# Kernel tuning notes

Hardware: AMD Instinct MI355X
Metric: run time of the kernel (lower is better)

The kernel has to match this reference:

```python
import jax, jax.numpy as jnp
import numpy as np

B, L, D = 4, 2048, 2048
NH, HD, K = 32, 64, 16
LR = 1.0
EPS = 1e-6


def ln_fwd(x, gamma, beta):
    mu = x.mean(-1, keepdims=True)
    var = jnp.var(x, axis=-1, keepdims=True)
    x_hat = (x - mu) / jnp.sqrt(var + EPS)
    return gamma * x_hat + beta


def ln_fused_l2_bwd(x, target, gamma, beta):
    # grad of 0.5*||LN(x)-target||^2 wrt x (matches LayerNormFunction.backward
    # with grad_output = LN(x) - target)
    d = x.shape[-1]
    mu = x.mean(-1, keepdims=True)
    var = jnp.var(x, axis=-1, keepdims=True)
    std = jnp.sqrt(var + EPS)
    x_hat = (x - mu) / std
    y = gamma * x_hat + beta
    g = (y - target) * gamma
    return (d * g - g.sum(-1, keepdims=True) - x_hat * (g * x_hat).sum(-1, keepdims=True)) / (d * std)


def setup_inputs() -> dict:
    key = jax.random.key(0)
    ks = jax.random.split(key, 12)
    s = 0.02
    return {
        "hidden_states": jax.random.normal(ks[0], (B, L, D), jnp.float32),
        "Wq": jax.random.normal(ks[1], (D, D), jnp.float32) * s,
        "Wk": jax.random.normal(ks[2], (D, D), jnp.float32) * s,
        "Wv": jax.random.normal(ks[3], (D, D), jnp.float32) * s,
        "Wo": jax.random.normal(ks[4], (D, D), jnp.float32) * s,
        "linear_weight": jax.random.normal(ks[5], (NH, 1, D), jnp.float32) * s,
        "linear_bias": jnp.zeros((NH, 1), jnp.float32),
        "ln_weight": jnp.ones((NH, HD), jnp.float32),
        "ln_bias": jnp.zeros((NH, HD), jnp.float32),
        "W1_init": jax.random.normal(ks[6], (NH, HD, HD), jnp.float32) * s,
        "b1_init": jnp.zeros((NH, 1, HD), jnp.float32),
    }


def reference(hidden_states, Wq, Wk, Wv, Wo, linear_weight, linear_bias,
              ln_weight, ln_bias, W1_init, b1_init):
    Bq, Lq, Dq = hidden_states.shape
    n_chunk = Lq // K

    def split(x):  # [B,L,D] -> [B,NH,n_chunk,K,HD]
        return x.reshape(Bq, n_chunk, K, NH, HD).transpose(0, 3, 1, 2, 4)

    XC = split(hidden_states @ Wq.T)
    XB = split(hidden_states @ Wk.T)
    XA = split(hidden_states @ Wv.T)

    # inner-loop learning-rate coefficient: [B,NH,n_chunk,K,1]
    X = hidden_states.reshape(Bq, n_chunk, K, Dq)
    ilr = jnp.einsum('bnkd,hd->bhnk', X, linear_weight[:, 0, :]) + linear_bias[:, 0][None, :, None, None]
    ilr_gated = jax.nn.sigmoid(ilr)[..., None]
    token_idx = 1.0 / jnp.arange(1, K + 1, dtype=hidden_states.dtype)
    coeff = (LR * token_idx).reshape(1, 1, 1, K, 1) * ilr_gated / HD

    ln_w = ln_weight.reshape(1, NH, 1, HD)
    ln_b = ln_bias.reshape(1, NH, 1, HD)
    mask = jnp.tril(jnp.ones((K, K), hidden_states.dtype))

    W1 = jnp.broadcast_to(W1_init[None], (Bq, NH, HD, HD))
    b1 = jnp.broadcast_to(b1_init[None], (Bq, NH, 1, HD))

    def step(carry, inp):
        W1, b1 = carry
        xc, xb, xa, co = inp  # [B,NH,K,HD], co: [B,NH,K,1]
        Z1 = xb @ W1 + b1
        grad = ln_fused_l2_bwd(Z1, xa - xb, ln_w, ln_b)  # [B,NH,K,HD]
        Attn = mask * jnp.einsum('bhkf,bhjf->bhkj', xc, xb)
        E = mask * co.transpose(0, 1, 3, 2)  # E[i,j] = coeff_j * (j<=i)
        b1_bar = b1 - E @ grad
        Z1_bar = xc @ W1 - (Attn * E) @ grad + b1_bar
        W1_new = W1 - jnp.einsum('bhkf,bhkg->bhfg', co * xb, grad)
        b1_new = b1 - (co * grad).sum(-2, keepdims=True)
        out = xc + ln_fwd(Z1_bar, ln_w, ln_b)
        return (W1_new, b1_new), out

    xs = (XC.transpose(2, 0, 1, 3, 4), XB.transpose(2, 0, 1, 3, 4),
          XA.transpose(2, 0, 1, 3, 4), coeff.transpose(2, 0, 1, 3, 4))
    (_, _), outs = jax.lax.scan(step, (W1, b1), xs)
    # outs: [n_chunk,B,NH,K,HD] -> [B,L,D]
    XCW = outs.transpose(1, 0, 3, 2, 4).reshape(Bq, Lq, Dq)
    return XCW @ Wo.T
```

## Files before the change

kernel.cpp:

```cpp
#include <hip/hip_runtime.h>


typedef __attribute__((ext_vector_type(4))) float float4v;
typedef __attribute__((ext_vector_type(2))) float float2v;
typedef __attribute__((ext_vector_type(8))) __bf16 bf16x8;
typedef __attribute__((ext_vector_type(4))) short short4v;
typedef __attribute__((ext_vector_type(4))) unsigned int uint4v;
typedef __attribute__((ext_vector_type(2))) unsigned int uint2v;

__device__ __forceinline__ unsigned short f2bf(float f) {
  unsigned int u = __builtin_bit_cast(unsigned int, f);
  u += 0x7FFFu + ((u >> 16) & 1u);
  return (unsigned short)(u >> 16);
}
__device__ __forceinline__ float bf2f(unsigned short s) {
  unsigned int u = ((unsigned int)s) << 16;
  return __builtin_bit_cast(float, u);
}
__device__ __forceinline__ void lds_load16(const void* g, void* l) {
  __builtin_amdgcn_global_load_lds((const __attribute__((address_space(1))) void*)g,
                                   (__attribute__((address_space(3))) void*)l, 16, 0, 0);
}

__device__ __forceinline__ void store_out(float* p, float v) { *p = v; }
__device__ __forceinline__ void store_out(unsigned short* p, float v) { *p = f2bf(v); }

template <int CTRL>
__device__ __forceinline__ float dppmov(float x) {
  return __builtin_bit_cast(
      float, __builtin_amdgcn_update_dpp(0, __builtin_bit_cast(int, x), CTRL, 0xF, 0xF, true));
}
__device__ __forceinline__ float red16(float x) {
  x += dppmov<0xB1>(x);
  x += dppmov<0x4E>(x);
  x += dppmov<0x124>(x);
  x += dppmov<0x128>(x);
  return x;
}
__device__ __forceinline__ unsigned int cvtpk_bf16(float lo, float hi) {
  unsigned int r;
  asm("v_cvt_pk_bf16_f32 %0, %1, %2" : "=v"(r) : "v"(lo), "v"(hi));
  return r;
}
__device__ __forceinline__ void bar_sync() {
  asm volatile("s_waitcnt lgkmcnt(0)" ::: "memory");
  __builtin_amdgcn_s_barrier();
  asm volatile("" ::: "memory");
}

template <typename OUT>
__global__ __launch_bounds__(256) void gemm_bt(
    const unsigned short* __restrict__ A, const unsigned short* __restrict__ B,
    OUT* __restrict__ C, int M, int N, int K) {
  __shared__ unsigned short sA[128 * 32];
  __shared__ unsigned short sB[128 * 32];
  const int tid = threadIdx.x;
  const int wave = tid >> 6;
  const int lane = tid & 63;
  const int quad = lane >> 4;
  const int l15 = lane & 15;
  const int wm = (wave >> 1) * 64;
  const int wn = (wave & 1) * 64;
  const int bm = blockIdx.y * 128;
  const int bn = blockIdx.x * 128;

  float4v acc[4][4];
#pragma unroll
  for (int i = 0; i < 4; ++i)
#pragma unroll
    for (int j = 0; j < 4; ++j) acc[i][j] = (float4v){0.f, 0.f, 0.f, 0.f};

  const int srow = tid >> 2;
  const int scol = (tid & 3) * 8;
  const unsigned short* aptr = A + (size_t)(bm + srow) * K + scol;
  const unsigned short* bptr = B + (size_t)(bn + srow) * K + scol;
  unsigned short* sAw0 = &sA[wave * 512];
  unsigned short* sAw1 = &sA[2048 + wave * 512];
  unsigned short* sBw0 = &sB[wave * 512];
  unsigned short* sBw1 = &sB[2048 + wave * 512];
  const size_t astep = (size_t)64 * K;

  for (int kt = 0; kt < K; kt += 32) {
    __syncthreads();
    lds_load16(aptr + kt, sAw0);
    lds_load16(aptr + kt + astep, sAw1);
    lds_load16(bptr + kt, sBw0);
    lds_load16(bptr + kt + astep, sBw1);
    __syncthreads();
    bf16x8 af[4], bf[4];
#pragma unroll
    for (int i = 0; i < 4; ++i)
      af[i] = *(const bf16x8*)&sA[(wm + i * 16 + l15) * 32 + quad * 8];
#pragma unroll
    for (int j = 0; j < 4; ++j)
      bf[j] = *(const bf16x8*)&sB[(wn + j * 16 + l15) * 32 + quad * 8];
#pragma unroll
    for (int i = 0; i < 4; ++i)
#pragma unroll
      for (int j = 0; j < 4; ++j)
        acc[i][j] = __builtin_amdgcn_mfma_f32_16x16x32_bf16(af[i], bf[j], acc[i][j], 0, 0, 0);
  }

#pragma unroll
  for (int i = 0; i < 4; ++i) {
    const int row0 = bm + wm + i * 16 + quad * 4;
#pragma unroll
    for (int j = 0; j < 4; ++j) {
      const int col = bn + wn + j * 16 + l15;
#pragma unroll
      for (int r = 0; r < 4; ++r)
        store_out(&C[(size_t)(row0 + r) * N + col], acc[i][j][r]);
    }
  }
}

__global__ __launch_bounds__(256) void f32_to_bf16_k(const float* __restrict__ s,
                                                     unsigned short* __restrict__ d, int n) {
  const int i = (blockIdx.x * 256 + threadIdx.x) * 8;
  if (i >= n) return;
  const float4v a = *(const float4v*)(s + i);
  const float4v b = *(const float4v*)(s + i + 4);
  uint4v o;
  o[0] = (unsigned int)f2bf(a[0]) | ((unsigned int)f2bf(a[1]) << 16);
  o[1] = (unsigned int)f2bf(a[2]) | ((unsigned int)f2bf(a[3]) << 16);
  o[2] = (unsigned int)f2bf(b[0]) | ((unsigned int)f2bf(b[1]) << 16);
  o[3] = (unsigned int)f2bf(b[2]) | ((unsigned int)f2bf(b[3]) << 16);
  *(uint4v*)(d + i) = o;
}

__global__ __launch_bounds__(256) void coeff_k(const unsigned short* __restrict__ ilr,
                                               const float* __restrict__ lb,
                                               float* __restrict__ coeff) {
  const int gid = blockIdx.x * 256 + threadIdx.x;
  const int row = gid >> 5;
  const int h = gid & 31;
  const float v = bf2f(ilr[row * 128 + h]) + lb[h];
  const float sig = 1.0f / (1.0f + __expf(-v));
  const int b = row >> 11;
  const int pos = row & 2047;
  const int cc = pos >> 4;
  const int k = pos & 15;
  coeff[((((size_t)b * 32 + h) * 128 + cc) << 4) + k] = sig / (64.0f * (float)(k + 1));
}

__global__ __launch_bounds__(256, 1) void ttt_scan(
    const unsigned short* __restrict__ XC, const unsigned short* __restrict__ XB,
    const unsigned short* __restrict__ XA, const float* __restrict__ coeff,
    const float* __restrict__ lnw, const float* __restrict__ lnb,
    const float* __restrict__ W1i, const float* __restrict__ b1i,
    unsigned short* __restrict__ XCW) {
  const int b = blockIdx.x >> 5;
  const int h = blockIdx.x & 31;
  const int tid = threadIdx.x;
  const int wave = tid >> 6;
  const int lane = tid & 63;
  const int quad = lane >> 4;
  const int l15 = lane & 15;

  constexpr int LDW = 88;
  __shared__ __attribute__((aligned(16))) unsigned short sXC[2][16 * LDW];
  __shared__ __attribute__((aligned(16))) unsigned short sXB[2][16 * LDW];
  __shared__ __attribute__((aligned(16))) unsigned short sXA[2][16 * LDW];
  __shared__ __attribute__((aligned(16))) unsigned short sW1[64 * LDW];
  __shared__ __attribute__((aligned(16))) float sRed[3][16][8];

  const int fcol = wave * 16 + l15;
  const float gam = lnw[h * 64 + fcol];
  const float bet = lnb[h * 64 + fcol];

  float4v W1r[4];
#pragma unroll
  for (int mt = 0; mt < 4; ++mt) {
    float4v v;
#pragma unroll
    for (int r = 0; r < 4; ++r)
      v[r] = W1i[(size_t)h * 4096 + (size_t)(mt * 16 + quad * 4 + r) * 64 + fcol];
    W1r[mt] = v;
  }
  float b1v = b1i[h * 64 + fcol];

#pragma unroll
  for (int mt = 0; mt < 4; ++mt) {
    uint2v p;
    p[0] = cvtpk_bf16(W1r[mt][0], W1r[mt][1]);
    p[1] = cvtpk_bf16(W1r[mt][2], W1r[mt][3]);
    *(uint2v*)&sW1[(size_t)fcol * LDW + mt * 16 + quad * 4] = p;
  }

  const int u = tid & 127;
  const int grow = u >> 3;
  const int gcol = (u & 7) * 8;
  const size_t hdoff = (size_t)h * 64;
  const size_t browoff = (size_t)b * 2048;
  const float* cobase = coeff + (((size_t)b * 32 + h) * 128) * 16;
  const float inv64 = 1.0f / 64.0f;
  const float4v zero4 = {0.f, 0.f, 0.f, 0.f};

  uint4v pA = {0, 0, 0, 0}, pB = {0, 0, 0, 0};
  float4v pcof;
  {
    const size_t goff = (browoff + (size_t)grow) * 2048 + hdoff + gcol;
    if (tid < 128) {
      pA = *(const uint4v*)(XC + goff);
      pB = *(const uint4v*)(XA + goff);
    } else {
      pA = *(const uint4v*)(XB + goff);
    }
    pcof = *(const float4v*)(cobase + quad * 4);
  }

  for (int c = 0; c < 128; ++c) {
    const int buf = c & 1;
    if (tid < 128) {
      *(uint4v*)&sXC[buf][grow * LDW + gcol] = pA;
      *(uint4v*)&sXA[buf][grow * LDW + gcol] = pB;
    } else {
      *(uint4v*)&sXB[buf][grow * LDW + gcol] = pA;
    }
    const float4v cof = pcof;
    bar_sync();

    {
      const int cn = (c < 127) ? c + 1 : 127;
      const size_t goff = (browoff + (size_t)(cn * 16 + grow)) * 2048 + hdoff + gcol;
      if (tid < 128) {
        pA = *(const uint4v*)(XC + goff);
        pB = *(const uint4v*)(XA + goff);
      } else {
        pA = *(const uint4v*)(XB + goff);
      }
      pcof = *(const float4v*)(cobase + (size_t)cn * 16 + quad * 4);
    }

    bf16x8 xbf[2], xcf[2], w1f[2];
#pragma unroll
    for (int hh = 0; hh < 2; ++hh) {
      xbf[hh] = *(const bf16x8*)&sXB[buf][l15 * LDW + hh * 32 + quad * 8];
      xcf[hh] = *(const bf16x8*)&sXC[buf][l15 * LDW + hh * 32 + quad * 8];
      w1f[hh] = *(const bf16x8*)&sW1[(size_t)fcol * LDW + hh * 32 + quad * 8];
    }

    float4v z = __builtin_amdgcn_mfma_f32_16x16x32_bf16(xbf[0], w1f[0], zero4, 0, 0, 0);
    z = __builtin_amdgcn_mfma_f32_16x16x32_bf16(xbf[1], w1f[1], z, 0, 0, 0);
#pragma unroll
    for (int r = 0; r < 4; ++r) z[r] += b1v;

    float s1p[4], s2p[4];
#pragma unroll
    for (int r = 0; r < 4; ++r) {
      s1p[r] = red16(z[r]);
      s2p[r] = red16(z[r] * z[r]);
    }
    if (l15 == 0) {
#pragma unroll
      for (int r = 0; r < 4; ++r)
        *(float2v*)&sRed[0][quad * 4 + r][wave * 2] = (float2v){s1p[r], s2p[r]};
    }

    float4v at = __builtin_amdgcn_mfma_f32_16x16x32_bf16(xbf[0], xcf[0], zero4, 0, 0, 0);
    at = __builtin_amdgcn_mfma_f32_16x16x32_bf16(xbf[1], xcf[1], at, 0, 0, 0);

    bar_sync();

    float mu[4], rstd[4];
#pragma unroll
    for (int r = 0; r < 4; ++r) {
      const float4v v0 = *(const float4v*)&sRed[0][quad * 4 + r][0];
      const float4v v1 = *(const float4v*)&sRed[0][quad * 4 + r][4];
      const float s1 = v0[0] + v0[2] + v1[0] + v1[2];
      const float s2 = v0[1] + v0[3] + v1[1] + v1[3];
      mu[r] = s1 * inv64;
      rstd[r] = rsqrtf(s2 * inv64 - mu[r] * mu[r] + 1e-6f);
    }
    float xh[4], gg[4];
#pragma unroll
    for (int r = 0; r < 4; ++r) {
      xh[r] = (z[r] - mu[r]) * rstd[r];
      const int toff = (quad * 4 + r) * LDW + fcol;
      const float tgt = bf2f(sXA[buf][toff]) - bf2f(sXB[buf][toff]);
      gg[r] = (gam * xh[r] + bet - tgt) * gam;
    }
    float sgp[4], sgxp[4];
#pragma unroll
    for (int r = 0; r < 4; ++r) {
      sgp[r] = red16(gg[r]);
      sgxp[r] = red16(gg[r] * xh[r]);
    }
    if (l15 == 0) {
#pragma unroll
      for (int r = 0; r < 4; ++r)
        *(float2v*)&sRed[1][quad * 4 + r][wave * 2] = (float2v){sgp[r], sgxp[r]};
    }

    short4v caf[4];
#pragma unroll
    for (int mt = 0; mt < 4; ++mt)
#pragma unroll
      for (int jj = 0; jj < 4; ++jj)
        caf[mt][jj] =
            (short)f2bf(-cof[jj] * bf2f(sXB[buf][(quad * 4 + jj) * LDW + mt * 16 + l15]));
    short4v m1f;
#pragma unroll
    for (int jj = 0; jj < 4; ++jj) {
      const int k = quad * 4 + jj;
      const float e = (k <= l15) ? cof[jj] : 0.0f;
      m1f[jj] = (short)f2bf(-(at[jj] + 1.0f) * e);
    }

    bar_sync();

    float grad[4];
    short4v gradb;
#pragma unroll
    for (int r = 0; r < 4; ++r) {
      const float4v v0 = *(const float4v*)&sRed[1][quad * 4 + r][0];
      const float4v v1 = *(const float4v*)&sRed[1][quad * 4 + r][4];
      const float sg = v0[0] + v0[2] + v1[0] + v1[2];
      const float sgx = v0[1] + v0[3] + v1[1] + v1[3];
      grad[r] = (64.0f * gg[r] - sg - xh[r] * sgx) * (rstd[r] * inv64);
      gradb[r] = (short)f2bf(grad[r]);
    }

    float4v zb = __builtin_amdgcn_mfma_f32_16x16x32_bf16(xcf[0], w1f[0], zero4, 0, 0, 0);
    zb = __builtin_amdgcn_mfma_f32_16x16x32_bf16(xcf[1], w1f[1], zb, 0, 0, 0);
    zb = __builtin_amdgcn_mfma_f32_16x16x16bf16_1k(m1f, gradb, zb, 0, 0, 0);
#pragma unroll
    for (int r = 0; r < 4; ++r) zb[r] += b1v;

#pragma unroll
    for (int r = 0; r < 4; ++r) {
      s1p[r] = red16(zb[r]);
      s2p[r] = red16(zb[r] * zb[r]);
    }
    if (l15 == 0) {
#pragma unroll
      for (int r = 0; r < 4; ++r)
        *(float2v*)&sRed[2][quad * 4 + r][wave * 2] = (float2v){s1p[r], s2p[r]};
    }

    {
      float pb = cof[0] * grad[0] + cof[1] * grad[1] + cof[2] * grad[2] + cof[3] * grad[3];
      pb += __shfl_xor(pb, 16);
      pb += __shfl_xor(pb, 32);
      b1v -= pb;
    }
#pragma unroll
    for (int mt = 0; mt < 4; ++mt)
      W1r[mt] = __builtin_amdgcn_mfma_f32_16x16x16bf16_1k(caf[mt], gradb, W1r[mt], 0, 0, 0);

    bar_sync();

#pragma unroll
    for (int r = 0; r < 4; ++r) {
      const float4v v0 = *(const float4v*)&sRed[2][quad * 4 + r][0];
      const float4v v1 = *(const float4v*)&sRed[2][quad * 4 + r][4];
      const float s1 = v0[0] + v0[2] + v1[0] + v1[2];
      const float s2 = v0[1] + v0[3] + v1[1] + v1[3];
      const float mu2 = s1 * inv64;
      const float rstd2 = rsqrtf(s2 * inv64 - mu2 * mu2 + 1e-6f);
      const float xhat = (zb[r] - mu2) * rstd2;
      const float y = gam * xhat + bet;
      const float o = bf2f(sXC[buf][(quad * 4 + r) * LDW + fcol]) + y;
      XCW[(browoff + (size_t)(c * 16 + quad * 4 + r)) * 2048 + hdoff + fcol] = f2bf(o);
    }

#pragma unroll
    for (int mt = 0; mt < 4; ++mt) {
      uint2v p;
      p[0] = cvtpk_bf16(W1r[mt][0], W1r[mt][1]);
      p[1] = cvtpk_bf16(W1r[mt][2], W1r[mt][3]);
      *(uint2v*)&sW1[(size_t)fcol * LDW + mt * 16 + quad * 4] = p;
    }
  }
}

extern "C" void kernel_launch(void* const* d_in, const int* in_sizes, int n_in,
                              void* d_out, int out_size, void* d_ws, size_t ws_size,
                              hipStream_t stream) {
  const float* hs = (const float*)d_in[0];
  const float* Wq = (const float*)d_in[1];
  const float* Wk = (const float*)d_in[2];
  const float* Wv = (const float*)d_in[3];
  const float* Wo = (const float*)d_in[4];
  const float* lw = (const float*)d_in[5];
  const float* lb = (const float*)d_in[6];
  const float* lnw = (const float*)d_in[7];
  const float* lnb = (const float*)d_in[8];
  const float* W1i = (const float*)d_in[9];
  const float* b1i = (const float*)d_in[10];
  float* out = (float*)d_out;
  char* ws = (char*)d_ws;

  unsigned short* hsb = (unsigned short*)(ws);
  unsigned short* wqb = (unsigned short*)(ws + 33554432);
  unsigned short* wkb = (unsigned short*)(ws + 41943040);
  unsigned short* wvb = (unsigned short*)(ws + 50331648);
  unsigned short* wob = (unsigned short*)(ws + 58720256);
  unsigned short* lwb = (unsigned short*)(ws + 67108864);
  unsigned short* XCb = (unsigned short*)(ws + 67633152);
  unsigned short* XBb = (unsigned short*)(ws + 101187584);
  unsigned short* XAb = (unsigned short*)(ws + 134742016);
  unsigned short* ilrb = (unsigned short*)(ws + 168296448);
  float* coeff = (float*)(ws + 170393600);

  f32_to_bf16_k<<<8192, 256, 0, stream>>>(hs, hsb, 16777216);
  f32_to_bf16_k<<<2048, 256, 0, stream>>>(Wq, wqb, 4194304);
  f32_to_bf16_k<<<2048, 256, 0, stream>>>(Wk, wkb, 4194304);
  f32_to_bf16_k<<<2048, 256, 0, stream>>>(Wv, wvb, 4194304);
  f32_to_bf16_k<<<2048, 256, 0, stream>>>(Wo, wob, 4194304);
  hipMemsetAsync(lwb, 0, 524288, stream);
  f32_to_bf16_k<<<32, 256, 0, stream>>>(lw, lwb, 65536);

  dim3 blk(256);
  dim3 gbig(16, 64);
  gemm_bt<unsigned short><<<gbig, blk, 0, stream>>>(hsb, wqb, XCb, 8192, 2048, 2048);
  gemm_bt<unsigned short><<<gbig, blk, 0, stream>>>(hsb, wkb, XBb, 8192, 2048, 2048);
  gemm_bt<unsigned short><<<gbig, blk, 0, stream>>>(hsb, wvb, XAb, 8192, 2048, 2048);
  gemm_bt<unsigned short><<<dim3(1, 64), blk, 0, stream>>>(hsb, lwb, ilrb, 8192, 128, 2048);
  coeff_k<<<1024, 256, 0, stream>>>(ilrb, lb, coeff);
  ttt_scan<<<128, 256, 0, stream>>>(XCb, XBb, XAb, coeff, lnw, lnb, W1i, b1i, hsb);
  gemm_bt<float><<<gbig, blk, 0, stream>>>(hsb, wob, out, 8192, 2048, 2048);
}
```

Before: 926.1 us.

## Double-buffer LDS tiles in bf16 GEMM to overlap global loads with MFMA

The GEMM kernel now keeps two LDS buffers for the A and B tiles and prefetches the next k-tile with global_load_lds while MFMAs run on the current one. This replaces the two barriers per iteration with a single wait-and-barrier at the end, hiding global load latency. LDS use doubles to 32KB per block, which may reduce occupancy. Correctness depends on the vmcnt wait plus barrier ordering the async LDS writes against other waves' reads.

```diff
diff --git a/kernel.cpp b/kernel.cpp
--- a/kernel.cpp
+++ b/kernel.cpp
@@ -47,13 +47,18 @@
   __builtin_amdgcn_s_barrier();
   asm volatile("" ::: "memory");
 }
+__device__ __forceinline__ void vm_bar() {
+  asm volatile("s_waitcnt vmcnt(0)" ::: "memory");
+  __builtin_amdgcn_s_barrier();
+  asm volatile("" ::: "memory");
+}
 
 template <typename OUT>
 __global__ __launch_bounds__(256) void gemm_bt(
     const unsigned short* __restrict__ A, const unsigned short* __restrict__ B,
     OUT* __restrict__ C, int M, int N, int K) {
-  __shared__ unsigned short sA[128 * 32];
-  __shared__ unsigned short sB[128 * 32];
+  __shared__ unsigned short sA[2][128 * 32];
+  __shared__ unsigned short sB[2][128 * 32];
   const int tid = threadIdx.x;
   const int wave = tid >> 6;
   const int lane = tid & 63;
@@ -74,31 +79,38 @@
   const int scol = (tid & 3) * 8;
   const unsigned short* aptr = A + (size_t)(bm + srow) * K + scol;
   const unsigned short* bptr = B + (size_t)(bn + srow) * K + scol;
-  unsigned short* sAw0 = &sA[wave * 512];
-  unsigned short* sAw1 = &sA[2048 + wave * 512];
-  unsigned short* sBw0 = &sB[wave * 512];
-  unsigned short* sBw1 = &sB[2048 + wave * 512];
   const size_t astep = (size_t)64 * K;
-
+  const int woff = wave * 512;
+
+  lds_load16(aptr, &sA[0][woff]);
+  lds_load16(aptr + astep, &sA[0][2048 + woff]);
+  lds_load16(bptr, &sB[0][woff]);
+  lds_load16(bptr + astep, &sB[0][2048 + woff]);
+  vm_bar();
+
+  int cur = 0;
   for (int kt = 0; kt < K; kt += 32) {
-    __syncthreads();
-    lds_load16(aptr + kt, sAw0);
-    lds_load16(aptr + kt + astep, sAw1);
-    lds_load16(bptr + kt, sBw0);
-    lds_load16(bptr + kt + astep, sBw1);
-    __syncthreads();
+    if (kt + 32 < K) {
+      const int nxt = cur ^ 1;
+      lds_load16(aptr + kt + 32, &sA[nxt][woff]);
+      lds_load16(aptr + kt + 32 + astep, &sA[nxt][2048 + woff]);
+      lds_load16(bptr + kt + 32, &sB[nxt][woff]);
+      lds_load16(bptr + kt + 32 + astep, &sB[nxt][2048 + woff]);
+    }
     bf16x8 af[4], bf[4];
 #pragma unroll
     for (int i = 0; i < 4; ++i)
-      af[i] = *(const bf16x8*)&sA[(wm + i * 16 + l15) * 32 + quad * 8];
+      af[i] = *(const bf16x8*)&sA[cur][(wm + i * 16 + l15) * 32 + quad * 8];
 #pragma unroll
     for (int j = 0; j < 4; ++j)
-      bf[j] = *(const bf16x8*)&sB[(wn + j * 16 + l15) * 32 + quad * 8];
+      bf[j] = *(const bf16x8*)&sB[cur][(wn + j * 16 + l15) * 32 + quad * 8];
 #pragma unroll
     for (int i = 0; i < 4; ++i)
 #pragma unroll
       for (int j = 0; j < 4; ++j)
         acc[i][j] = __builtin_amdgcn_mfma_f32_16x16x32_bf16(af[i], bf[j], acc[i][j], 0, 0, 0);
+    vm_bar();
+    cur ^= 1;
   }
 
 #pragma unroll
```

Result: faster. 872.0 us (-5.8%).
